# Kernel optimization log

Measured on AMD Instinct MI355X. Metric: run time of the kernel, lower is better.

The kernel has to match this reference:

```python
import jax, jax.numpy as jnp
import numpy as np

VOCAB = 128
HID = 1024
STD = 0.01


def setup_inputs() -> dict:
    key = jax.random.key(0)
    ks = jax.random.split(key, 9)
    X = jax.random.randint(ks[0], (64, 512), 0, VOCAB, dtype=jnp.int32)
    def w(k, shape):
        return jax.random.normal(k, shape, dtype=jnp.float32) * STD
    return {
        "X": X,
        # reset gate
        "Wr_x": w(ks[1], (VOCAB, HID)), "Wr_h": w(ks[2], (HID, HID)), "b_r": jnp.zeros(HID, jnp.float32),
        # update gate
        "Wz_x": w(ks[3], (VOCAB, HID)), "Wz_h": w(ks[4], (HID, HID)), "b_z": jnp.zeros(HID, jnp.float32),
        # candidate
        "Wh_x": w(ks[5], (VOCAB, HID)), "Wh_h": w(ks[6], (HID, HID)), "b_h": jnp.zeros(HID, jnp.float32),
        # output head
        "W_o": w(ks[7], (HID, VOCAB)), "b_o": jnp.zeros(VOCAB, jnp.float32),
    }


def reference(X, Wr_x, Wr_h, b_r, Wz_x, Wz_h, b_z, Wh_x, Wh_h, b_h, W_o, b_o):
    B, T = X.shape
    # one-hot encode all timesteps: (T, B, V)
    Xoh = jax.nn.one_hot(X.T, VOCAB, dtype=jnp.float32)

    def step(h, x_t):
        # x_t: (B, V), h: (B, H)
        r = jax.nn.sigmoid(x_t @ Wr_x + h @ Wr_h + b_r)
        z = jax.nn.sigmoid(x_t @ Wz_x + h @ Wz_h + b_z)
        h_tilde = jnp.tanh(x_t @ Wh_x + (r * h) @ Wh_h + b_h)
        h_new = z * h + (1.0 - z) * h_tilde
        out = h_new @ W_o + b_o  # (B, V)
        return h_new, out

    h0 = jnp.zeros((B, HID), jnp.float32)
    _, outs = jax.lax.scan(step, h0, Xoh)  # outs: (T, B, V)
    return jnp.transpose(outs, (1, 0, 2))  # (B, T, V)
```

## Files before the change

### kernel.cpp

```cpp
#include <hip/hip_runtime.h>

#define HID   1024
#define TLEN  512
#define VOC   128
#define NBLK  256
#define NW    32
#define NO    2
#define LDSK  1032
#define HBUF  (64 * HID)
#define OD    16

typedef __bf16 bf16_t;
typedef __attribute__((ext_vector_type(8))) __bf16 bf16x8;
typedef __attribute__((ext_vector_type(4))) float  f32x4;
typedef __attribute__((ext_vector_type(2))) float  f32x2;
typedef __attribute__((ext_vector_type(4))) unsigned uint4v;

__device__ __forceinline__ float sigmoid_fast(float x) {
  return 1.0f / (1.0f + __expf(-x));
}
__device__ __forceinline__ float tanh_fast(float x) {
  float e = __expf(-2.0f * x);
  return (1.0f - e) / (1.0f + e);
}

union PairU { bf16_t b[2]; unsigned u; };

__device__ __forceinline__ void l1_inv() {
  asm volatile("buffer_inv" ::: "memory");
}

__device__ __forceinline__ void st_sc1(bf16_t* p, float f0, float f1) {
  PairU c; c.b[0] = (bf16_t)f0; c.b[1] = (bf16_t)f1;
  __hip_atomic_store((unsigned*)p, c.u, __ATOMIC_RELAXED, __HIP_MEMORY_SCOPE_AGENT);
}
__device__ __forceinline__ bf16x8 ld_nt16(const bf16_t* p) {
  union { uint4v u; bf16x8 b; } c;
  c.u = __builtin_nontemporal_load((const uint4v*)p);
  return c.b;
}

__device__ __forceinline__ void wait1(const unsigned* ctr, unsigned tgt) {
  if (threadIdx.x == 0) {
    while (__hip_atomic_load(ctr, __ATOMIC_RELAXED, __HIP_MEMORY_SCOPE_AGENT) < tgt)
      __builtin_amdgcn_s_sleep(1);
  }
  __syncthreads();
}

__device__ __forceinline__ void wait_rh_oc(const unsigned* rctr, const unsigned* oc0,
                                           const unsigned* oc1, unsigned tgt, unsigned otgt) {
  if (threadIdx.x < 64) {
    const int lane = threadIdx.x;
    for (;;) {
      bool ok = true;
      if (lane == 0)      ok = __hip_atomic_load(rctr, __ATOMIC_RELAXED, __HIP_MEMORY_SCOPE_AGENT) >= tgt;
      else if (lane == 1) ok = __hip_atomic_load(oc0,  __ATOMIC_RELAXED, __HIP_MEMORY_SCOPE_AGENT) >= otgt;
      else if (lane == 2) ok = __hip_atomic_load(oc1,  __ATOMIC_RELAXED, __HIP_MEMORY_SCOPE_AGENT) >= otgt;
      if (__all(ok)) break;
      __builtin_amdgcn_s_sleep(1);
    }
  }
  __syncthreads();
}

__device__ __forceinline__ void publish_add(unsigned* ctr) {
  __syncthreads();
  if (threadIdx.x == 0)
    __hip_atomic_fetch_add(ctr, 1u, __ATOMIC_RELAXED, __HIP_MEMORY_SCOPE_AGENT);
}
__device__ __forceinline__ void publish_val(unsigned* f, unsigned v) {
  __syncthreads();
  if (threadIdx.x == 0)
    __hip_atomic_store(f, v, __ATOMIC_RELAXED, __HIP_MEMORY_SCOPE_AGENT);
}

#define MFMA(a, b, c) __builtin_amdgcn_mfma_f32_16x16x32_bf16((a), (b), (c), 0, 0, 0)

__global__ void __launch_bounds__(256, 1)
gru_ctr(const int* __restrict__ X,
        const float* __restrict__ Wr_x, const float* __restrict__ Wr_h, const float* __restrict__ b_r,
        const float* __restrict__ Wz_x, const float* __restrict__ Wz_h, const float* __restrict__ b_z,
        const float* __restrict__ Wh_x, const float* __restrict__ Wh_h, const float* __restrict__ b_h,
        const float* __restrict__ W_o,  const float* __restrict__ b_o,
        float* __restrict__ out,
        bf16_t* __restrict__ hring, bf16_t* __restrict__ rh_bf,
        bf16_t* __restrict__ oring, bf16_t* __restrict__ wz_bf,
        unsigned* __restrict__ flags)
{
  __shared__ __align__(16) bf16_t Wbuf[2 * 32 * LDSK];
  __shared__ int s_role;

  unsigned* h_ctr  = flags;
  unsigned* rh_ctr = flags + 32;
  unsigned* oc0    = flags + 64;
  unsigned* oc1    = flags + 96;
  unsigned* cnt    = flags + 128;
  unsigned* winner = flags + 160;
  unsigned* ocnt   = flags + 164;

  const int tid  = threadIdx.x;
  const int lane = tid & 63;
  const int wv   = tid >> 6;
  const int n16  = lane & 15;
  const int q    = lane >> 4;
  const int aoff = (wv * 16 + n16) * HID + q * 8;

  int bi[4];
#pragma unroll
  for (int i = 0; i < 4; ++i) bi[i] = wv * 16 + q * 4 + i;

  if (tid == 0) {
    unsigned xcc;
    asm volatile("s_getreg_b32 %0, hwreg(HW_REG_XCC_ID)" : "=s"(xcc));
    xcc &= 7u;
    unsigned idx = __hip_atomic_fetch_add(&cnt[xcc], 1u, __ATOMIC_RELAXED, __HIP_MEMORY_SCOPE_AGENT);
    if (idx == NW - 1) {
      unsigned exp = 0u;
      __hip_atomic_compare_exchange_strong(winner, &exp, xcc + 1u,
          __ATOMIC_RELAXED, __ATOMIC_RELAXED, __HIP_MEMORY_SCOPE_AGENT);
    }
    unsigned w;
    do {
      w = __hip_atomic_load(winner, __ATOMIC_RELAXED, __HIP_MEMORY_SCOPE_AGENT);
      __builtin_amdgcn_s_sleep(1);
    } while (w == 0u);
    if (xcc == w - 1u && idx < NW) {
      s_role = (int)idx;
    } else {
      unsigned o = __hip_atomic_fetch_add(ocnt, 1u, __ATOMIC_RELAXED, __HIP_MEMORY_SCOPE_AGENT);
      s_role = (o < NO) ? (NW + (int)o) : -1;
    }
  }
  __syncthreads();
  const int role = s_role;
  if (role < 0) return;

  if (role < NW) {
    const int s  = role;
    const int c0 = s * 32;
    for (int idx = tid; idx < 32 * HID; idx += 256) {
      int n = idx & 31, k = idx >> 5;
      int r = (n & 1) * 16 + (n >> 1);
      Wbuf[r * LDSK + k]             = (bf16_t)Wr_h[k * HID + c0 + n];
      Wbuf[32 * LDSK + r * LDSK + k] = (bf16_t)Wh_h[k * HID + c0 + n];
    }
    bf16_t* wzs = wz_bf + s * (32 * 1024);
    for (int idx = tid; idx < 32 * HID; idx += 256) {
      int n = idx & 31, k = idx >> 5;
      int r = (n & 1) * 16 + (n >> 1);
      wzs[r * 1024 + k] = (bf16_t)Wz_h[k * HID + c0 + n];
    }

    const int j0 = c0 + 2 * n16;
#pragma unroll
    for (int i = 0; i < 4; ++i) {
      PairU zz; zz.b[0] = (bf16_t)0.f; zz.b[1] = (bf16_t)0.f;
      *reinterpret_cast<PairU*>(hring + bi[i] * HID + j0) = zz;
    }
    publish_add(h_ctr);

    const float br0 = b_r[j0], br1 = b_r[j0 + 1];
    const float bz0 = b_z[j0], bz1 = b_z[j0 + 1];
    const float bh0 = b_h[j0], bh1 = b_h[j0 + 1];
    const bf16_t* wr0 = &Wbuf[n16 * LDSK + q * 8];
    const bf16_t* wr1 = &Wbuf[(16 + n16) * LDSK + q * 8];
    const bf16_t* wh0 = &Wbuf[32 * LDSK + n16 * LDSK + q * 8];
    const bf16_t* wh1 = &Wbuf[32 * LDSK + (16 + n16) * LDSK + q * 8];
    const bf16_t* wz0 = wzs + n16 * 1024 + q * 8;
    const bf16_t* wz1 = wzs + (16 + n16) * 1024 + q * 8;
    const bf16_t* rhrow = rh_bf + aoff;

    f32x4 hm0 = {0.f,0.f,0.f,0.f}, hm1 = {0.f,0.f,0.f,0.f};

    for (int t = 0; t < TLEN; ++t) {
      float gr0[4], gr1[4], gz0[4], gz1[4], gh0[4], gh1[4];
#pragma unroll
      for (int i = 0; i < 4; ++i) {
        int xb = X[bi[i] * TLEN + t];
        gr0[i] = Wr_x[xb * HID + j0]; gr1[i] = Wr_x[xb * HID + j0 + 1];
        gz0[i] = Wz_x[xb * HID + j0]; gz1[i] = Wz_x[xb * HID + j0 + 1];
        gh0[i] = Wh_x[xb * HID + j0]; gh1[i] = Wh_x[xb * HID + j0 + 1];
      }
      wait1(h_ctr, (unsigned)(NW * (t + 1)));
      l1_inv();
      const bf16_t* hslot = hring + (t & 1) * HBUF;
      const bf16_t* hrow  = hslot + aoff;
      bf16x8 areg[32];
#pragma unroll
      for (int kk = 0; kk < 32; ++kk)
        areg[kk] = *reinterpret_cast<const bf16x8*>(hrow + kk * 32);
      f32x4 aR0 = {0.f,0.f,0.f,0.f}, aR1 = {0.f,0.f,0.f,0.f};
#pragma unroll
      for (int kk = 0; kk < 32; ++kk) {
        bf16x8 w0 = *reinterpret_cast<const bf16x8*>(wr0 + kk * 32);
        bf16x8 w1 = *reinterpret_cast<const bf16x8*>(wr1 + kk * 32);
        aR0 = MFMA(areg[kk], w0, aR0);
        aR1 = MFMA(areg[kk], w1, aR1);
      }
#pragma unroll
      for (int i = 0; i < 4; ++i) {
        float r0 = sigmoid_fast(aR0[i] + br0 + gr0[i]);
        float r1 = sigmoid_fast(aR1[i] + br1 + gr1[i]);
        PairU hp = *reinterpret_cast<const PairU*>(hslot + bi[i] * HID + j0);
        PairU c;
        c.b[0] = (bf16_t)(r0 * (float)hp.b[0]);
        c.b[1] = (bf16_t)(r1 * (float)hp.b[1]);
        *reinterpret_cast<PairU*>(rh_bf + bi[i] * HID + j0) = c;
      }
      publish_add(rh_ctr);

      f32x4 aZ0 = {0.f,0.f,0.f,0.f}, aZ1 = {0.f,0.f,0.f,0.f};
#pragma unroll
      for (int kk = 0; kk < 32; ++kk) {
        bf16x8 w0 = *reinterpret_cast<const bf16x8*>(wz0 + kk * 32);
        bf16x8 w1 = *reinterpret_cast<const bf16x8*>(wz1 + kk * 32);
        aZ0 = MFMA(areg[kk], w0, aZ0);
        aZ1 = MFMA(areg[kk], w1, aZ1);
      }
      f32x4 z0, z1;
#pragma unroll
      for (int i = 0; i < 4; ++i) {
        z0[i] = sigmoid_fast(aZ0[i] + bz0 + gz0[i]);
        z1[i] = sigmoid_fast(aZ1[i] + bz1 + gz1[i]);
      }

      unsigned otgt = (t > OD - 1) ? (unsigned)(t + 1 - OD) : 0u;
      wait_rh_oc(rh_ctr, oc0, oc1, (unsigned)(NW * (t + 1)), otgt);
      l1_inv();
      bf16x8 breg[32];
#pragma unroll
      for (int kk = 0; kk < 32; ++kk)
        breg[kk] = *reinterpret_cast<const bf16x8*>(rhrow + kk * 32);
      f32x4 aH0 = {0.f,0.f,0.f,0.f}, aH1 = {0.f,0.f,0.f,0.f};
#pragma unroll
      for (int kk = 0; kk < 32; ++kk) {
        bf16x8 w0 = *reinterpret_cast<const bf16x8*>(wh0 + kk * 32);
        bf16x8 w1 = *reinterpret_cast<const bf16x8*>(wh1 + kk * 32);
        aH0 = MFMA(breg[kk], w0, aH0);
        aH1 = MFMA(breg[kk], w1, aH1);
      }
      bf16_t* hnext = hring + ((t + 1) & 1) * HBUF;
      bf16_t* onext = oring + ((t + 1) % OD) * HBUF;
#pragma unroll
      for (int i = 0; i < 4; ++i) {
        float ht0 = tanh_fast(aH0[i] + bh0 + gh0[i]);
        float ht1 = tanh_fast(aH1[i] + bh1 + gh1[i]);
        float hn0 = z0[i] * hm0[i] + (1.f - z0[i]) * ht0;
        float hn1 = z1[i] * hm1[i] + (1.f - z1[i]) * ht1;
        hm0[i] = hn0; hm1[i] = hn1;
        PairU c; c.b[0] = (bf16_t)hn0; c.b[1] = (bf16_t)hn1;
        *reinterpret_cast<PairU*>(hnext + bi[i] * HID + j0) = c;
        st_sc1(onext + bi[i] * HID + j0, hn0, hn1);
      }
      publish_add(h_ctr);
    }
    __builtin_amdgcn_fence(__ATOMIC_RELEASE, "agent");
  } else {
    const int ob  = role - NW;
    const int c0o = ob * 64;
    for (int idx = tid; idx < 64 * HID; idx += 256) {
      int n = idx & 63, k = idx >> 6;
      int g = n >> 5, m = n & 31;
      int r = g * 32 + (m & 1) * 16 + (m >> 1);
      Wbuf[r * LDSK + k] = (bf16_t)W_o[k * VOC + c0o + n];
    }
    __syncthreads();

    float bo[2][2];
#pragma unroll
    for (int g = 0; g < 2; ++g) {
      bo[g][0] = b_o[c0o + 32 * g + 2 * n16];
      bo[g][1] = b_o[c0o + 32 * g + 2 * n16 + 1];
    }
    const bf16_t* wo[2][2];
#pragma unroll
    for (int g = 0; g < 2; ++g)
#pragma unroll
      for (int h = 0; h < 2; ++h)
        wo[g][h] = &Wbuf[(g * 32 + h * 16 + n16) * LDSK + q * 8];

    unsigned* myoc = (ob == 0) ? oc0 : oc1;
    for (int t = 1; t <= TLEN; ++t) {
      wait1(h_ctr, (unsigned)(NW * (t + 1)));
      const bf16_t* hrow = oring + (t % OD) * HBUF + aoff;
      bf16x8 areg[32];
#pragma unroll
      for (int kk = 0; kk < 32; ++kk)
        areg[kk] = ld_nt16(hrow + kk * 32);
      f32x4 acc[2][2];
#pragma unroll
      for (int g = 0; g < 2; ++g)
#pragma unroll
        for (int h = 0; h < 2; ++h)
          acc[g][h] = (f32x4){0.f, 0.f, 0.f, 0.f};
#pragma unroll
      for (int kk = 0; kk < 32; ++kk) {
#pragma unroll
        for (int g = 0; g < 2; ++g) {
          bf16x8 w0 = *reinterpret_cast<const bf16x8*>(wo[g][0] + kk * 32);
          bf16x8 w1 = *reinterpret_cast<const bf16x8*>(wo[g][1] + kk * 32);
          acc[g][0] = MFMA(areg[kk], w0, acc[g][0]);
          acc[g][1] = MFMA(areg[kk], w1, acc[g][1]);
        }
      }
#pragma unroll
      for (int g = 0; g < 2; ++g) {
        const int j0 = c0o + 32 * g + 2 * n16;
#pragma unroll
        for (int i = 0; i < 4; ++i) {
          f32x2 v = {acc[g][0][i] + bo[g][0], acc[g][1][i] + bo[g][1]};
          *reinterpret_cast<f32x2*>(&out[(bi[i] * TLEN + (t - 1)) * VOC + j0]) = v;
        }
      }
      publish_val(myoc, (unsigned)t);
    }
  }
}

extern "C" void kernel_launch(void* const* d_in, const int* in_sizes, int n_in,
                              void* d_out, int out_size, void* d_ws, size_t ws_size,
                              hipStream_t stream) {
  const int*   X    = (const int*)d_in[0];
  const float* Wr_x = (const float*)d_in[1];
  const float* Wr_h = (const float*)d_in[2];
  const float* b_r  = (const float*)d_in[3];
  const float* Wz_x = (const float*)d_in[4];
  const float* Wz_h = (const float*)d_in[5];
  const float* b_z  = (const float*)d_in[6];
  const float* Wh_x = (const float*)d_in[7];
  const float* Wh_h = (const float*)d_in[8];
  const float* b_h  = (const float*)d_in[9];
  const float* W_o  = (const float*)d_in[10];
  const float* b_o  = (const float*)d_in[11];

  char* ws = (char*)d_ws;
  unsigned* flags = (unsigned*)ws;
  bf16_t*   hring = (bf16_t*)(ws + 4096);
  bf16_t*   rh_bf = (bf16_t*)(ws + 4096 + 2 * HBUF * sizeof(bf16_t));
  bf16_t*   oring = (bf16_t*)(ws + 4096 + 3 * HBUF * sizeof(bf16_t));
  bf16_t*   wz_bf = (bf16_t*)(ws + 4096 + (3 + OD) * HBUF * sizeof(bf16_t));

  hipMemsetAsync(ws, 0, 4096, stream);

  gru_ctr<<<NBLK, 256, 0, stream>>>(
      X, Wr_x, Wr_h, b_r, Wz_x, Wz_h, b_z, Wh_x, Wh_h, b_h, W_o, b_o,
      (float*)d_out, hring, rh_bf, oring, wz_bf, flags);
}
```

Measured before the change: 8.425 ms.

## Replace atomic counter barriers with per-block local flag arrays polled via L2

Replaces the global atomic-counter barriers between the 32 recurrent blocks with per-block flag words. Each block writes its own flag with a volatile store, and waiters poll all 32 flags in one wavefront after invalidating L1. Fetch_add contention on a single counter goes away, and the sleep-based polling on the h and rh barriers is replaced by busy polling. The output-head backpressure check now runs only every 8 steps, and a startup barrier makes sure all recurrent blocks are resident. The release ordering of the plain volatile stores is weaker, which risks memory-ordering bugs.

```diff
diff --git a/kernel.cpp b/kernel.cpp
--- a/kernel.cpp
+++ b/kernel.cpp
@@ -40,6 +40,35 @@
   return c.b;
 }
 
+__device__ __forceinline__ void wait_local(const unsigned* lfl, int n, unsigned tgt) {
+  if ((threadIdx.x >> 6) == 0) {
+    const int lane = threadIdx.x & 63;
+    for (;;) {
+      l1_inv();
+      unsigned g = tgt;
+      if (lane < n)
+        g = *(volatile const unsigned*)&lfl[lane];
+      if (__all(g >= tgt)) break;
+    }
+  }
+  __syncthreads();
+}
+
+__device__ __forceinline__ void wait_out_mall(const unsigned* oc0, const unsigned* oc1,
+                                              unsigned otgt) {
+  if ((threadIdx.x >> 6) == 0) {
+    const int lane = threadIdx.x & 63;
+    for (;;) {
+      bool ok = true;
+      if (lane == 0)      ok = __hip_atomic_load(oc0, __ATOMIC_RELAXED, __HIP_MEMORY_SCOPE_AGENT) >= otgt;
+      else if (lane == 1) ok = __hip_atomic_load(oc1, __ATOMIC_RELAXED, __HIP_MEMORY_SCOPE_AGENT) >= otgt;
+      if (__all(ok)) break;
+      __builtin_amdgcn_s_sleep(1);
+    }
+  }
+  __syncthreads();
+}
+
 __device__ __forceinline__ void wait1(const unsigned* ctr, unsigned tgt) {
   if (threadIdx.x == 0) {
     while (__hip_atomic_load(ctr, __ATOMIC_RELAXED, __HIP_MEMORY_SCOPE_AGENT) < tgt)
@@ -48,37 +77,10 @@
   __syncthreads();
 }
 
-__device__ __forceinline__ void wait_rh_oc(const unsigned* rctr, const unsigned* oc0,
-                                           const unsigned* oc1, unsigned tgt, unsigned otgt) {
-  if (threadIdx.x < 64) {
-    const int lane = threadIdx.x;
-    for (;;) {
-      bool ok = true;
-      if (lane == 0)      ok = __hip_atomic_load(rctr, __ATOMIC_RELAXED, __HIP_MEMORY_SCOPE_AGENT) >= tgt;
-      else if (lane == 1) ok = __hip_atomic_load(oc0,  __ATOMIC_RELAXED, __HIP_MEMORY_SCOPE_AGENT) >= otgt;
-      else if (lane == 2) ok = __hip_atomic_load(oc1,  __ATOMIC_RELAXED, __HIP_MEMORY_SCOPE_AGENT) >= otgt;
-      if (__all(ok)) break;
-      __builtin_amdgcn_s_sleep(1);
-    }
-  }
-  __syncthreads();
-}
-
-__device__ __forceinline__ void publish_add(unsigned* ctr) {
-  __syncthreads();
-  if (threadIdx.x == 0)
-    __hip_atomic_fetch_add(ctr, 1u, __ATOMIC_RELAXED, __HIP_MEMORY_SCOPE_AGENT);
-}
-__device__ __forceinline__ void publish_val(unsigned* f, unsigned v) {
-  __syncthreads();
-  if (threadIdx.x == 0)
-    __hip_atomic_store(f, v, __ATOMIC_RELAXED, __HIP_MEMORY_SCOPE_AGENT);
-}
-
 #define MFMA(a, b, c) __builtin_amdgcn_mfma_f32_16x16x32_bf16((a), (b), (c), 0, 0, 0)
 
 __global__ void __launch_bounds__(256, 1)
-gru_ctr(const int* __restrict__ X,
+gru_lfl(const int* __restrict__ X,
         const float* __restrict__ Wr_x, const float* __restrict__ Wr_h, const float* __restrict__ b_r,
         const float* __restrict__ Wz_x, const float* __restrict__ Wz_h, const float* __restrict__ b_z,
         const float* __restrict__ Wh_x, const float* __restrict__ Wh_h, const float* __restrict__ b_h,
@@ -86,18 +88,21 @@
         float* __restrict__ out,
         bf16_t* __restrict__ hring, bf16_t* __restrict__ rh_bf,
         bf16_t* __restrict__ oring, bf16_t* __restrict__ wz_bf,
-        unsigned* __restrict__ flags)
+        unsigned* __restrict__ flags, unsigned* __restrict__ lflags)
 {
   __shared__ __align__(16) bf16_t Wbuf[2 * 32 * LDSK];
   __shared__ int s_role;
 
   unsigned* h_ctr  = flags;
-  unsigned* rh_ctr = flags + 32;
   unsigned* oc0    = flags + 64;
   unsigned* oc1    = flags + 96;
   unsigned* cnt    = flags + 128;
   unsigned* winner = flags + 160;
   unsigned* ocnt   = flags + 164;
+  unsigned* winv   = flags + 168;
+
+  unsigned* lhf = lflags;
+  unsigned* lrf = lflags + 64;
 
   const int tid  = threadIdx.x;
   const int lane = tid & 63;
@@ -137,6 +142,14 @@
   if (role < 0) return;
 
   if (role < NW) {
+    __builtin_amdgcn_fence(__ATOMIC_ACQUIRE, "agent");
+    if (tid == 0) {
+      __hip_atomic_fetch_add(winv, 1u, __ATOMIC_RELAXED, __HIP_MEMORY_SCOPE_AGENT);
+      while (__hip_atomic_load(winv, __ATOMIC_RELAXED, __HIP_MEMORY_SCOPE_AGENT) < NW)
+        __builtin_amdgcn_s_sleep(1);
+    }
+    __syncthreads();
+
     const int s  = role;
     const int c0 = s * 32;
     for (int idx = tid; idx < 32 * HID; idx += 256) {
@@ -158,7 +171,11 @@
       PairU zz; zz.b[0] = (bf16_t)0.f; zz.b[1] = (bf16_t)0.f;
       *reinterpret_cast<PairU*>(hring + bi[i] * HID + j0) = zz;
     }
-    publish_add(h_ctr);
+    __syncthreads();
+    if (tid == 0) {
+      *(volatile unsigned*)&lhf[s] = 1u;
+      __hip_atomic_fetch_add(h_ctr, 1u, __ATOMIC_RELAXED, __HIP_MEMORY_SCOPE_AGENT);
+    }
 
     const float br0 = b_r[j0], br1 = b_r[j0 + 1];
     const float bz0 = b_z[j0], bz1 = b_z[j0 + 1];
@@ -182,8 +199,7 @@
         gz0[i] = Wz_x[xb * HID + j0]; gz1[i] = Wz_x[xb * HID + j0 + 1];
         gh0[i] = Wh_x[xb * HID + j0]; gh1[i] = Wh_x[xb * HID + j0 + 1];
       }
-      wait1(h_ctr, (unsigned)(NW * (t + 1)));
-      l1_inv();
+      wait_local(lhf, NW, (unsigned)(t + 1));
       const bf16_t* hslot = hring + (t & 1) * HBUF;
       const bf16_t* hrow  = hslot + aoff;
       bf16x8 areg[32];
@@ -208,7 +224,8 @@
         c.b[1] = (bf16_t)(r1 * (float)hp.b[1]);
         *reinterpret_cast<PairU*>(rh_bf + bi[i] * HID + j0) = c;
       }
-      publish_add(rh_ctr);
+      __syncthreads();
+      if (tid == 0) *(volatile unsigned*)&lrf[s] = (unsigned)(t + 1);
 
       f32x4 aZ0 = {0.f,0.f,0.f,0.f}, aZ1 = {0.f,0.f,0.f,0.f};
 #pragma unroll
@@ -225,9 +242,9 @@
         z1[i] = sigmoid_fast(aZ1[i] + bz1 + gz1[i]);
       }
 
-      unsigned otgt = (t > OD - 1) ? (unsigned)(t + 1 - OD) : 0u;
-      wait_rh_oc(rh_ctr, oc0, oc1, (unsigned)(NW * (t + 1)), otgt);
-      l1_inv();
+      if ((t & 7) == 0 && t + 8 > OD)
+        wait_out_mall(oc0, oc1, (unsigned)(t + 8 - OD));
+      wait_local(lrf, NW, (unsigned)(t + 1));
       bf16x8 breg[32];
 #pragma unroll
       for (int kk = 0; kk < 32; ++kk)
@@ -253,7 +270,11 @@
         *reinterpret_cast<PairU*>(hnext + bi[i] * HID + j0) = c;
         st_sc1(onext + bi[i] * HID + j0, hn0, hn1);
       }
-      publish_add(h_ctr);
+      __syncthreads();
+      if (tid == 0) {
+        *(volatile unsigned*)&lhf[s] = (unsigned)(t + 2);
+        __hip_atomic_fetch_add(h_ctr, 1u, __ATOMIC_RELAXED, __HIP_MEMORY_SCOPE_AGENT);
+      }
     }
     __builtin_amdgcn_fence(__ATOMIC_RELEASE, "agent");
   } else {
@@ -313,7 +334,9 @@
           *reinterpret_cast<f32x2*>(&out[(bi[i] * TLEN + (t - 1)) * VOC + j0]) = v;
         }
       }
-      publish_val(myoc, (unsigned)t);
+      __syncthreads();
+      if (tid == 0)
+        __hip_atomic_store(myoc, (unsigned)t, __ATOMIC_RELAXED, __HIP_MEMORY_SCOPE_AGENT);
     }
   }
 }
@@ -335,15 +358,16 @@
   const float* b_o  = (const float*)d_in[11];
 
   char* ws = (char*)d_ws;
-  unsigned* flags = (unsigned*)ws;
-  bf16_t*   hring = (bf16_t*)(ws + 4096);
-  bf16_t*   rh_bf = (bf16_t*)(ws + 4096 + 2 * HBUF * sizeof(bf16_t));
-  bf16_t*   oring = (bf16_t*)(ws + 4096 + 3 * HBUF * sizeof(bf16_t));
-  bf16_t*   wz_bf = (bf16_t*)(ws + 4096 + (3 + OD) * HBUF * sizeof(bf16_t));
-
-  hipMemsetAsync(ws, 0, 4096, stream);
-
-  gru_ctr<<<NBLK, 256, 0, stream>>>(
+  unsigned* flags  = (unsigned*)ws;
+  unsigned* lflags = (unsigned*)(ws + 4096);
+  bf16_t*   hring  = (bf16_t*)(ws + 8192);
+  bf16_t*   rh_bf  = (bf16_t*)(ws + 8192 + 2 * HBUF * sizeof(bf16_t));
+  bf16_t*   oring  = (bf16_t*)(ws + 8192 + 3 * HBUF * sizeof(bf16_t));
+  bf16_t*   wz_bf  = (bf16_t*)(ws + 8192 + (3 + OD) * HBUF * sizeof(bf16_t));
+
+  hipMemsetAsync(ws, 0, 8192, stream);
+
+  gru_lfl<<<NBLK, 256, 0, stream>>>(
       X, Wr_x, Wr_h, b_r, Wz_x, Wz_h, b_z, Wh_x, Wh_h, b_h, W_o, b_o,
-      (float*)d_out, hring, rh_bf, oring, wz_bf, flags);
-}
+      (float*)d_out, hring, rh_bf, oring, wz_bf, flags, lflags);
+}
```

Result: slower. 8.606 ms (+2.1%).
